# Kernel tuning notes

Measured on AMD Instinct MI355X. Metric: run time of the kernel, lower is better.

## Reference

```python
import jax, jax.numpy as jnp
import numpy as np

N_NODES = 50000
N_EDGES = 800000
D = 64
BN_EPS = 1e-5


def setup_inputs() -> dict:
    key = jax.random.key(0)
    ks = jax.random.split(key, 16)
    x = jax.random.normal(ks[0], (N_NODES, D), dtype=jnp.float32)
    edge_index = jax.random.randint(ks[1], (2, N_EDGES), 0, N_NODES, dtype=jnp.int64)
    s = 1.0 / np.sqrt(D)
    def lin(k):
        kw, kb = jax.random.split(k)
        W = jax.random.uniform(kw, (D, D), jnp.float32, -s, s)
        b = jax.random.uniform(kb, (D,), jnp.float32, -s, s)
        return W, b
    W1_0, b1_0 = lin(ks[2])
    W2_0, b2_0 = lin(ks[3])
    W1_1, b1_1 = lin(ks[4])
    W2_1, b2_1 = lin(ks[5])
    return {
        "x": x, "edge_index": edge_index,
        "W1_0": W1_0, "b1_0": b1_0, "g_0": jnp.ones((D,), jnp.float32), "beta_0": jnp.zeros((D,), jnp.float32), "W2_0": W2_0, "b2_0": b2_0,
        "W1_1": W1_1, "b1_1": b1_1, "g_1": jnp.ones((D,), jnp.float32), "beta_1": jnp.zeros((D,), jnp.float32), "W2_1": W2_1, "b2_1": b2_1,
    }


def _gin_layer(x, src, dst, W1, b1, g, beta, W2, b2):
    # GINConv with eps=0: h_i = MLP( x_i + sum_{j->i} x_j )
    agg = jax.ops.segment_sum(x[src], dst, num_segments=N_NODES)  # [N, D]
    h = agg + x
    h = h @ W1 + b1
    # BatchNorm1d (training-mode batch statistics, biased variance)
    mean = jnp.mean(h, axis=0)
    var = jnp.var(h, axis=0)
    h = (h - mean) * jax.lax.rsqrt(var + BN_EPS) * g + beta
    h = jax.nn.relu(h)
    h = jax.nn.relu(h @ W2 + b2)
    return h


def reference(x, edge_index, W1_0, b1_0, g_0, beta_0, W2_0, b2_0,
              W1_1, b1_1, g_1, beta_1, W2_1, b2_1):
    src = edge_index[0]  # message source j
    dst = edge_index[1]  # aggregation target i
    h1 = _gin_layer(x, src, dst, W1_0, b1_0, g_0, beta_0, W2_0, b2_0)
    h2 = _gin_layer(h1, src, dst, W1_1, b1_1, g_1, beta_1, W2_1, b2_1)
    return (h1, h2)
```

## Files before the change

### kernel.cpp

```cpp
#include <hip/hip_runtime.h>
#include <hip/hip_bf16.h>

#define N_NODES 50000
#define N_EDGES 800000
#define DD 64
#define RPB 64
#define GBLOCKS ((N_NODES + RPB - 1) / RPB)
#define MBLOCKS ((N_NODES + 63) / 64)
#define NBUCKET ((N_NODES + 63) / 64)
#define PIDSTRIDE 800
#define NBP (NBUCKET * 8)
#define EDGE_BLOCKS (N_EDGES / 256)
#define BN_EPS 1e-5f


__device__ __forceinline__ float bf2f(unsigned short b) {
    return __uint_as_float(((unsigned)b) << 16);
}
__device__ __forceinline__ float loadF(const void* p, int i, int isf) {
    return isf ? ((const float*)p)[i] : bf2f(((const unsigned short*)p)[i]);
}
template<bool ISF>
__device__ __forceinline__ float4 ld4(const void* p, int i) {
    if (ISF) return *reinterpret_cast<const float4*>((const float*)p + i);
    ushort4 u = *reinterpret_cast<const ushort4*>((const unsigned short*)p + i);
    return make_float4(bf2f(u.x), bf2f(u.y), bf2f(u.z), bf2f(u.w));
}
__device__ __forceinline__ void acc8(float4& a, float4& b, uint4 u) {
    a.x += __uint_as_float(u.x << 16);
    a.y += __uint_as_float(u.x & 0xFFFF0000u);
    a.z += __uint_as_float(u.y << 16);
    a.w += __uint_as_float(u.y & 0xFFFF0000u);
    b.x += __uint_as_float(u.z << 16);
    b.y += __uint_as_float(u.z & 0xFFFF0000u);
    b.z += __uint_as_float(u.w << 16);
    b.w += __uint_as_float(u.w & 0xFFFF0000u);
}

__global__ __launch_bounds__(256) void initcast_kernel(
    const void* __restrict__ x, const int* __restrict__ ei,
    int* __restrict__ flags, int* __restrict__ bpcnt,
    unsigned short* __restrict__ xb)
{
    __shared__ int cntF, cntI;
    int t = threadIdx.x;
    if (t == 0) { cntF = 0; cntI = 0; }
    __syncthreads();
    unsigned short wd = ((const unsigned short*)x)[2 * t];
    int e = (wd >> 7) & 0xFF;
    if (e >= 0x70 && e <= 0x8F) atomicAdd(&cntF, 1);
    if (t < 128 && ei[2 * t + 1] == 0) atomicAdd(&cntI, 1);
    __syncthreads();
    int isf = (cntF < 128) ? 1 : 0;
    int i64 = (cntI > 64) ? 1 : 0;

    int gid = blockIdx.x * 256 + t;
    if (blockIdx.x == 0 && t == 0) {
        flags[0] = isf;
        flags[1] = i64;
    }

    {
        int d = i64 ? ei[2 * N_EDGES + 2 * gid] : ei[N_EDGES + gid];
        atomicAdd(bpcnt + (blockIdx.x & 7) * PIDSTRIDE + (d >> 6), 1);
    }

    int i = gid * 8;
    if (i < N_NODES * DD) {
        if (isf) {
            float4 a = *reinterpret_cast<const float4*>((const float*)x + i);
            float4 b = *reinterpret_cast<const float4*>((const float*)x + i + 4);
            ushort4 o0, o1;
            o0.x = __bfloat16_as_ushort(__float2bfloat16(a.x));
            o0.y = __bfloat16_as_ushort(__float2bfloat16(a.y));
            o0.z = __bfloat16_as_ushort(__float2bfloat16(a.z));
            o0.w = __bfloat16_as_ushort(__float2bfloat16(a.w));
            o1.x = __bfloat16_as_ushort(__float2bfloat16(b.x));
            o1.y = __bfloat16_as_ushort(__float2bfloat16(b.y));
            o1.z = __bfloat16_as_ushort(__float2bfloat16(b.z));
            o1.w = __bfloat16_as_ushort(__float2bfloat16(b.w));
            *reinterpret_cast<ushort4*>(xb + i) = o0;
            *reinterpret_cast<ushort4*>(xb + i + 4) = o1;
        } else {
            *reinterpret_cast<uint4*>(xb + i) =
                *reinterpret_cast<const uint4*>((const unsigned short*)x + i);
        }
    }
}

#define BPCH 25
__global__ __launch_bounds__(256) void bpscan_kernel(const int* __restrict__ bpcnt,
                                                     int* __restrict__ bpcur,
                                                     int* __restrict__ boff) {
    __shared__ int tmp[256];
    int t = threadIdx.x;
    int lo = t * BPCH;
    int hi = lo + BPCH; if (hi > NBP) hi = NBP;
    int s = 0;
    for (int i = lo; i < hi; ++i)
        s += bpcnt[(i & 7) * PIDSTRIDE + (i >> 3)];
    tmp[t] = s;
    __syncthreads();
    #pragma unroll
    for (int d = 1; d < 256; d <<= 1) {
        int u = (t >= d) ? tmp[t - d] : 0;
        __syncthreads();
        tmp[t] += u;
        __syncthreads();
    }
    int run = (t == 0) ? 0 : tmp[t - 1];
    for (int i = lo; i < hi; ++i) {
        bpcur[i * 16] = run;
        if ((i & 7) == 0) boff[i >> 3] = run;
        run += bpcnt[(i & 7) * PIDSTRIDE + (i >> 3)];
    }
    if (t == 255) boff[NBUCKET] = tmp[255];
}

__global__ void fillA_kernel(const int* __restrict__ ei, int* __restrict__ bpcur,
                             unsigned int* __restrict__ tmp, const int* __restrict__ flags) {
    int i64 = flags[1];
    int e = blockIdx.x * 256 + threadIdx.x;
    int s, d;
    if (i64) { s = ei[2 * e]; d = ei[2 * N_EDGES + 2 * e]; }
    else     { s = ei[e];     d = ei[N_EDGES + e]; }
    int bin = (d >> 6) * 8 + (blockIdx.x & 7);
    int pos = atomicAdd(bpcur + bin * 16, 1);
    tmp[pos] = (unsigned)s | ((unsigned)(d & 63) << 16);
}

__global__ __launch_bounds__(256) void fillB_kernel(const int* __restrict__ boff,
                                                    const unsigned int* __restrict__ tmp,
                                                    unsigned short* __restrict__ srt,
                                                    int* __restrict__ off) {
    __shared__ int lcnt[64];
    __shared__ int cur64[64];
    int b = blockIdx.x;
    int t = threadIdx.x;
    if (t < 64) lcnt[t] = 0;
    __syncthreads();
    int start = boff[b], end = boff[b + 1];
    for (int i = start + t; i < end; i += 256)
        atomicAdd(&lcnt[tmp[i] >> 16], 1);
    __syncthreads();
    if (t < 64) {
        int v = lcnt[t];
        int s = v;
        #pragma unroll
        for (int d = 1; d < 64; d <<= 1) {
            int u = __shfl_up(s, d, 64);
            if (t >= d) s += u;
        }
        int o = start + (s - v);
        int node = b * 64 + t;
        if (node <= N_NODES) off[node] = o;
        cur64[t] = o;
    }
    __syncthreads();
    for (int i = start + t; i < end; i += 256) {
        unsigned v = tmp[i];
        int pos = atomicAdd(&cur64[v >> 16], 1);
        srt[pos] = (unsigned short)(v & 0xFFFFu);
    }
}

__global__ __launch_bounds__(512) void gather_gemm_stats_kernel(
    const unsigned short* __restrict__ xb, const void* __restrict__ self_src, int force_f32,
    const int* __restrict__ off, const unsigned short* __restrict__ srt,
    const void* __restrict__ W, const void* __restrict__ bias,
    float* __restrict__ out_, float* __restrict__ sums, const int* __restrict__ flags)
{
    __shared__ float sIn[RPB][DD];
    __shared__ float r1[8][DD], r2[8][DD];
    int tid = threadIdx.x;
    int lane = tid & 63, w = tid >> 6;
    int rs = lane >> 3, ch = lane & 7;
    int row0 = blockIdx.x * RPB;
    int isf = force_f32 ? 1 : flags[0];

    int lr = w * 8 + rs;
    int r = row0 + lr;
    float4 a  = make_float4(0.f, 0.f, 0.f, 0.f);
    float4 b  = make_float4(0.f, 0.f, 0.f, 0.f);
    float4 a2 = make_float4(0.f, 0.f, 0.f, 0.f);
    float4 b2 = make_float4(0.f, 0.f, 0.f, 0.f);
    if (r < N_NODES) {
        a = isf ? ld4<true>(self_src, r * DD + 8 * ch)
                : ld4<false>(self_src, r * DD + 8 * ch);
        b = isf ? ld4<true>(self_src, r * DD + 8 * ch + 4)
                : ld4<false>(self_src, r * DD + 8 * ch + 4);
        int k0 = off[r], k1 = off[r + 1];
        int k = k0;
        for (; k + 8 <= k1; k += 8) {
            int n0 = srt[k],     n1 = srt[k + 1], n2 = srt[k + 2], n3 = srt[k + 3];
            int n4 = srt[k + 4], n5 = srt[k + 5], n6 = srt[k + 6], n7 = srt[k + 7];
            uint4 u0 = *reinterpret_cast<const uint4*>(xb + n0 * DD + 8 * ch);
            uint4 u1 = *reinterpret_cast<const uint4*>(xb + n1 * DD + 8 * ch);
            uint4 u2 = *reinterpret_cast<const uint4*>(xb + n2 * DD + 8 * ch);
            uint4 u3 = *reinterpret_cast<const uint4*>(xb + n3 * DD + 8 * ch);
            uint4 u4 = *reinterpret_cast<const uint4*>(xb + n4 * DD + 8 * ch);
            uint4 u5 = *reinterpret_cast<const uint4*>(xb + n5 * DD + 8 * ch);
            uint4 u6 = *reinterpret_cast<const uint4*>(xb + n6 * DD + 8 * ch);
            uint4 u7 = *reinterpret_cast<const uint4*>(xb + n7 * DD + 8 * ch);
            acc8(a, b, u0);
            acc8(a2, b2, u1);
            acc8(a, b, u2);
            acc8(a2, b2, u3);
            acc8(a, b, u4);
            acc8(a2, b2, u5);
            acc8(a, b, u6);
            acc8(a2, b2, u7);
        }
        for (; k + 2 <= k1; k += 2) {
            int n0 = srt[k], n1 = srt[k + 1];
            uint4 u0 = *reinterpret_cast<const uint4*>(xb + n0 * DD + 8 * ch);
            uint4 u1 = *reinterpret_cast<const uint4*>(xb + n1 * DD + 8 * ch);
            acc8(a, b, u0);
            acc8(a2, b2, u1);
        }
        if (k < k1) {
            int n0 = srt[k];
            acc8(a, b, *reinterpret_cast<const uint4*>(xb + n0 * DD + 8 * ch));
        }
        a.x += a2.x; a.y += a2.y; a.z += a2.z; a.w += a2.w;
        b.x += b2.x; b.y += b2.y; b.z += b2.z; b.w += b2.w;
    }
    *reinterpret_cast<float4*>(&sIn[lr][8 * ch]) = a;
    *reinterpret_cast<float4*>(&sIn[lr][8 * ch + 4]) = b;
    __syncthreads();

    float wcol[DD];
    #pragma unroll
    for (int k = 0; k < DD; ++k) wcol[k] = loadF(W, k * DD + lane, isf);
    float bv = loadF(bias, lane, isf);

    float s1 = 0.f, s2 = 0.f;
    #pragma unroll 4
    for (int j = 0; j < 8; ++j) {
        int jr = w * 8 + j;
        float c0 = 0.f, c1 = 0.f, c2 = 0.f, c3 = 0.f;
        #pragma unroll
        for (int k = 0; k < DD; k += 4) {
            float4 aa = *reinterpret_cast<const float4*>(&sIn[jr][k]);
            c0 += aa.x * wcol[k];
            c1 += aa.y * wcol[k + 1];
            c2 += aa.z * wcol[k + 2];
            c3 += aa.w * wcol[k + 3];
        }
        float acc = bv + ((c0 + c1) + (c2 + c3));
        int rr = row0 + jr;
        if (rr < N_NODES) {
            out_[rr * DD + lane] = acc;
            s1 += acc;
            s2 += acc * acc;
        }
    }
    r1[w][lane] = s1; r2[w][lane] = s2;
    __syncthreads();
    if (w == 0) {
        float t1 = 0.f, t2 = 0.f;
        #pragma unroll
        for (int q = 0; q < 8; ++q) { t1 += r1[q][lane]; t2 += r2[q][lane]; }
        atomicAdd(&sums[lane], t1);
        atomicAdd(&sums[64 + lane], t2);
    }
}

__global__ __launch_bounds__(256) void mlp2_kernel(
    const float* __restrict__ in_, const float* __restrict__ sums,
    const void* __restrict__ gma, const void* __restrict__ beta,
    const void* __restrict__ W, const void* __restrict__ bias,
    float* __restrict__ oF, unsigned short* obf, const int* __restrict__ flags)
{
    __shared__ float sIn[64][DD];
    __shared__ float sScale[DD], sShift[DD];
    int isf = flags[0];
    int tid = threadIdx.x;
    int c = tid & 63, g = tid >> 6;
    int row0 = blockIdx.x * 64;

    if (tid < 64) {
        float S1 = sums[tid];
        float S2 = sums[64 + tid];
        float mean = S1 * (1.0f / N_NODES);
        float var  = S2 * (1.0f / N_NODES) - mean * mean;
        float scale = rsqrtf(var + BN_EPS) * loadF(gma, tid, isf);
        sScale[tid] = scale;
        sShift[tid] = loadF(beta, tid, isf) - mean * scale;
    }
    __syncthreads();

    #pragma unroll
    for (int j = 0; j < 4; ++j) {
        int lr = (tid >> 4) + 16 * j;
        int cc = (tid & 15) << 2;
        int r = row0 + lr;
        float4 v = make_float4(0.f, 0.f, 0.f, 0.f);
        if (r < N_NODES) {
            v = *reinterpret_cast<const float4*>(in_ + r * DD + cc);
            float4 sc = *reinterpret_cast<const float4*>(&sScale[cc]);
            float4 sh = *reinterpret_cast<const float4*>(&sShift[cc]);
            v.x = fmaxf(v.x * sc.x + sh.x, 0.f);
            v.y = fmaxf(v.y * sc.y + sh.y, 0.f);
            v.z = fmaxf(v.z * sc.z + sh.z, 0.f);
            v.w = fmaxf(v.w * sc.w + sh.w, 0.f);
        }
        *reinterpret_cast<float4*>(&sIn[lr][cc]) = v;
    }
    __syncthreads();

    float wcol[DD];
    #pragma unroll
    for (int k = 0; k < DD; ++k) wcol[k] = loadF(W, k * DD + c, isf);
    float bv = loadF(bias, c, isf);

    #pragma unroll 4
    for (int j = 0; j < 16; ++j) {
        int lr = g * 16 + j;
        float a0 = 0.f, a1 = 0.f, a2 = 0.f, a3 = 0.f;
        #pragma unroll
        for (int k = 0; k < DD; k += 4) {
            float4 a = *reinterpret_cast<const float4*>(&sIn[lr][k]);
            a0 += a.x * wcol[k];
            a1 += a.y * wcol[k + 1];
            a2 += a.z * wcol[k + 2];
            a3 += a.w * wcol[k + 3];
        }
        float acc = fmaxf(bv + ((a0 + a1) + (a2 + a3)), 0.f);
        int r = row0 + lr;
        if (r < N_NODES) {
            oF[r * DD + c] = acc;
            if (obf) obf[r * DD + c] = __bfloat16_as_ushort(__float2bfloat16(acc));
        }
    }
}

extern "C" void kernel_launch(void* const* d_in, const int* in_sizes, int n_in,
                              void* d_out, int out_size, void* d_ws, size_t ws_size,
                              hipStream_t stream)
{
    (void)in_sizes; (void)n_in; (void)out_size; (void)ws_size;
    const void* x  = d_in[0];
    const int* ei  = (const int*)d_in[1];
    const void* W1_0 = d_in[2];  const void* b1_0 = d_in[3];
    const void* g_0  = d_in[4];  const void* be_0 = d_in[5];
    const void* W2_0 = d_in[6];  const void* b2_0 = d_in[7];
    const void* W1_1 = d_in[8];  const void* b1_1 = d_in[9];
    const void* g_1  = d_in[10]; const void* be_1 = d_in[11];
    const void* W2_1 = d_in[12]; const void* b2_1 = d_in[13];

    float* wsf   = (float*)d_ws;
    float* sumsA = wsf;
    float* sumsB = wsf + 128;
    int*  flags  = (int*)(wsf + 256);
    int*  bpcnt  = (int*)(wsf + 512);
    int*  off    = bpcnt + 6400;
    int*  boff   = off + 50064;
    int*  bpcur  = boff + 800;
    unsigned int* tmp32 = (unsigned int*)(bpcur + 100096);
    unsigned short* srt = (unsigned short*)(tmp32 + 800000);
    unsigned short* xb  = srt + 800064;
    float* O1    = (float*)d_out;
    float* O2    = O1 + (size_t)N_NODES * DD;

    dim3 blk(256);

    hipMemsetAsync(d_ws, 0, (size_t)(512 + 6400) * 4, stream);
    initcast_kernel<<<EDGE_BLOCKS, blk, 0, stream>>>(x, ei, flags, bpcnt, xb);
    bpscan_kernel<<<1, blk, 0, stream>>>(bpcnt, bpcur, boff);
    fillA_kernel<<<EDGE_BLOCKS, blk, 0, stream>>>(ei, bpcur, tmp32, flags);
    fillB_kernel<<<NBUCKET, blk, 0, stream>>>(boff, tmp32, srt, off);

    gather_gemm_stats_kernel<<<GBLOCKS, 512, 0, stream>>>(xb, x, 0, off, srt, W1_0, b1_0,
                                                          O2, sumsA, flags);
    mlp2_kernel<<<MBLOCKS, blk, 0, stream>>>(O2, sumsA, g_0, be_0, W2_0, b2_0, O1, xb, flags);

    gather_gemm_stats_kernel<<<GBLOCKS, 512, 0, stream>>>(xb, O1, 1, off, srt, W1_1, b1_1,
                                                          O2, sumsB, flags);
    mlp2_kernel<<<MBLOCKS, blk, 0, stream>>>(O2, sumsB, g_1, be_1, W2_1, b2_1, O2, nullptr, flags);
}
```

Baseline: 309.2 us.

## Fuse per-bucket CSR fill into first-layer gather-GEMM-stats kernel

The second pass of the counting sort (per-bucket local histogram, scan and scatter into the sorted source array) now runs inside the first layer's gather/GEMM/BN-stats kernel, one block per 64-node bucket. This removes a kernel launch and the round trip through global memory for the row offsets, since the first layer reads them from shared memory. The cost is that each block must finish its sort before gathering. The freshly written srt values are then read back through the cache within the same block, and the larger block adds more sort threads. The second-layer kernel also drops the force_f32 flag and hardcodes float loads for its self input.

```diff
diff --git a/kernel.cpp b/kernel.cpp
--- a/kernel.cpp
+++ b/kernel.cpp
@@ -129,43 +129,146 @@
     tmp[pos] = (unsigned)s | ((unsigned)(d & 63) << 16);
 }
 
-__global__ __launch_bounds__(256) void fillB_kernel(const int* __restrict__ boff,
-                                                    const unsigned int* __restrict__ tmp,
-                                                    unsigned short* __restrict__ srt,
-                                                    int* __restrict__ off) {
-    __shared__ int lcnt[64];
-    __shared__ int cur64[64];
+__global__ __launch_bounds__(512) void gather1_fused_kernel(
+    const unsigned short* __restrict__ xb, const void* __restrict__ self_src,
+    const int* __restrict__ boff, const unsigned int* __restrict__ tmp,
+    unsigned short* __restrict__ srt, int* __restrict__ off,
+    const void* __restrict__ W, const void* __restrict__ bias,
+    float* __restrict__ out_, float* __restrict__ sums, const int* __restrict__ flags)
+{
+    __shared__ float sIn[RPB][DD];
+    __shared__ float r1[8][DD], r2[8][DD];
+    __shared__ int lofs[65];
+    int tid = threadIdx.x;
+    int lane = tid & 63, w = tid >> 6;
+    int rs = lane >> 3, ch = lane & 7;
     int b = blockIdx.x;
-    int t = threadIdx.x;
-    if (t < 64) lcnt[t] = 0;
-    __syncthreads();
-    int start = boff[b], end = boff[b + 1];
-    for (int i = start + t; i < end; i += 256)
-        atomicAdd(&lcnt[tmp[i] >> 16], 1);
-    __syncthreads();
-    if (t < 64) {
-        int v = lcnt[t];
-        int s = v;
+    int row0 = b * RPB;
+    int isf = flags[0];
+
+    {
+        int* lcnt = (int*)&r1[0][0];
+        int* cur  = lcnt + 64;
+        if (tid < 64) lcnt[tid] = 0;
+        __syncthreads();
+        int start = boff[b], end = boff[b + 1];
+        for (int i = start + tid; i < end; i += 512)
+            atomicAdd(&lcnt[tmp[i] >> 16], 1);
+        __syncthreads();
+        if (tid < 64) {
+            int v = lcnt[tid];
+            int s = v;
+            #pragma unroll
+            for (int d = 1; d < 64; d <<= 1) {
+                int u = __shfl_up(s, d, 64);
+                if (tid >= d) s += u;
+            }
+            int o = start + (s - v);
+            int node = row0 + tid;
+            if (node <= N_NODES) off[node] = o;
+            cur[tid] = o;
+            lofs[tid] = o;
+            if (tid == 63) lofs[64] = end;
+        }
+        __syncthreads();
+        for (int i = start + tid; i < end; i += 512) {
+            unsigned v = tmp[i];
+            int pos = atomicAdd(&cur[v >> 16], 1);
+            srt[pos] = (unsigned short)(v & 0xFFFFu);
+        }
+        __syncthreads();
+    }
+
+    int lr = w * 8 + rs;
+    int r = row0 + lr;
+    float4 a  = make_float4(0.f, 0.f, 0.f, 0.f);
+    float4 b4 = make_float4(0.f, 0.f, 0.f, 0.f);
+    float4 a2 = make_float4(0.f, 0.f, 0.f, 0.f);
+    float4 b2 = make_float4(0.f, 0.f, 0.f, 0.f);
+    if (r < N_NODES) {
+        a  = isf ? ld4<true>(self_src, r * DD + 8 * ch)
+                 : ld4<false>(self_src, r * DD + 8 * ch);
+        b4 = isf ? ld4<true>(self_src, r * DD + 8 * ch + 4)
+                 : ld4<false>(self_src, r * DD + 8 * ch + 4);
+        int k0 = lofs[lr], k1 = lofs[lr + 1];
+        int k = k0;
+        for (; k + 8 <= k1; k += 8) {
+            int n0 = srt[k],     n1 = srt[k + 1], n2 = srt[k + 2], n3 = srt[k + 3];
+            int n4 = srt[k + 4], n5 = srt[k + 5], n6 = srt[k + 6], n7 = srt[k + 7];
+            uint4 u0 = *reinterpret_cast<const uint4*>(xb + n0 * DD + 8 * ch);
+            uint4 u1 = *reinterpret_cast<const uint4*>(xb + n1 * DD + 8 * ch);
+            uint4 u2 = *reinterpret_cast<const uint4*>(xb + n2 * DD + 8 * ch);
+            uint4 u3 = *reinterpret_cast<const uint4*>(xb + n3 * DD + 8 * ch);
+            uint4 u4 = *reinterpret_cast<const uint4*>(xb + n4 * DD + 8 * ch);
+            uint4 u5 = *reinterpret_cast<const uint4*>(xb + n5 * DD + 8 * ch);
+            uint4 u6 = *reinterpret_cast<const uint4*>(xb + n6 * DD + 8 * ch);
+            uint4 u7 = *reinterpret_cast<const uint4*>(xb + n7 * DD + 8 * ch);
+            acc8(a, b4, u0);
+            acc8(a2, b2, u1);
+            acc8(a, b4, u2);
+            acc8(a2, b2, u3);
+            acc8(a, b4, u4);
+            acc8(a2, b2, u5);
+            acc8(a, b4, u6);
+            acc8(a2, b2, u7);
+        }
+        for (; k + 2 <= k1; k += 2) {
+            int n0 = srt[k], n1 = srt[k + 1];
+            uint4 u0 = *reinterpret_cast<const uint4*>(xb + n0 * DD + 8 * ch);
+            uint4 u1 = *reinterpret_cast<const uint4*>(xb + n1 * DD + 8 * ch);
+            acc8(a, b4, u0);
+            acc8(a2, b2, u1);
+        }
+        if (k < k1) {
+            int n0 = srt[k];
+            acc8(a, b4, *reinterpret_cast<const uint4*>(xb + n0 * DD + 8 * ch));
+        }
+        a.x += a2.x; a.y += a2.y; a.z += a2.z; a.w += a2.w;
+        b4.x += b2.x; b4.y += b2.y; b4.z += b2.z; b4.w += b2.w;
+    }
+    *reinterpret_cast<float4*>(&sIn[lr][8 * ch]) = a;
+    *reinterpret_cast<float4*>(&sIn[lr][8 * ch + 4]) = b4;
+    __syncthreads();
+
+    float wcol[DD];
+    #pragma unroll
+    for (int k = 0; k < DD; ++k) wcol[k] = loadF(W, k * DD + lane, isf);
+    float bv = loadF(bias, lane, isf);
+
+    float s1 = 0.f, s2 = 0.f;
+    #pragma unroll 4
+    for (int j = 0; j < 8; ++j) {
+        int jr = w * 8 + j;
+        float c0 = 0.f, c1 = 0.f, c2 = 0.f, c3 = 0.f;
         #pragma unroll
-        for (int d = 1; d < 64; d <<= 1) {
-            int u = __shfl_up(s, d, 64);
-            if (t >= d) s += u;
-        }
-        int o = start + (s - v);
-        int node = b * 64 + t;
-        if (node <= N_NODES) off[node] = o;
-        cur64[t] = o;
-    }
-    __syncthreads();
-    for (int i = start + t; i < end; i += 256) {
-        unsigned v = tmp[i];
-        int pos = atomicAdd(&cur64[v >> 16], 1);
-        srt[pos] = (unsigned short)(v & 0xFFFFu);
+        for (int k = 0; k < DD; k += 4) {
+            float4 aa = *reinterpret_cast<const float4*>(&sIn[jr][k]);
+            c0 += aa.x * wcol[k];
+            c1 += aa.y * wcol[k + 1];
+            c2 += aa.z * wcol[k + 2];
+            c3 += aa.w * wcol[k + 3];
+        }
+        float acc = bv + ((c0 + c1) + (c2 + c3));
+        int rr = row0 + jr;
+        if (rr < N_NODES) {
+            out_[rr * DD + lane] = acc;
+            s1 += acc;
+            s2 += acc * acc;
+        }
+    }
+    r1[w][lane] = s1; r2[w][lane] = s2;
+    __syncthreads();
+    if (w == 0) {
+        float t1 = 0.f, t2 = 0.f;
+        #pragma unroll
+        for (int q = 0; q < 8; ++q) { t1 += r1[q][lane]; t2 += r2[q][lane]; }
+        atomicAdd(&sums[lane], t1);
+        atomicAdd(&sums[64 + lane], t2);
     }
 }
 
 __global__ __launch_bounds__(512) void gather_gemm_stats_kernel(
-    const unsigned short* __restrict__ xb, const void* __restrict__ self_src, int force_f32,
+    const unsigned short* __restrict__ xb, const float* __restrict__ self_src,
     const int* __restrict__ off, const unsigned short* __restrict__ srt,
     const void* __restrict__ W, const void* __restrict__ bias,
     float* __restrict__ out_, float* __restrict__ sums, const int* __restrict__ flags)
@@ -176,7 +279,7 @@
     int lane = tid & 63, w = tid >> 6;
     int rs = lane >> 3, ch = lane & 7;
     int row0 = blockIdx.x * RPB;
-    int isf = force_f32 ? 1 : flags[0];
+    int isf = flags[0];
 
     int lr = w * 8 + rs;
     int r = row0 + lr;
@@ -185,10 +288,8 @@
     float4 a2 = make_float4(0.f, 0.f, 0.f, 0.f);
     float4 b2 = make_float4(0.f, 0.f, 0.f, 0.f);
     if (r < N_NODES) {
-        a = isf ? ld4<true>(self_src, r * DD + 8 * ch)
-                : ld4<false>(self_src, r * DD + 8 * ch);
-        b = isf ? ld4<true>(self_src, r * DD + 8 * ch + 4)
-                : ld4<false>(self_src, r * DD + 8 * ch + 4);
+        a = ld4<true>(self_src, r * DD + 8 * ch);
+        b = ld4<true>(self_src, r * DD + 8 * ch + 4);
         int k0 = off[r], k1 = off[r + 1];
         int k = k0;
         for (; k + 8 <= k1; k += 8) {
@@ -369,13 +470,12 @@
     initcast_kernel<<<EDGE_BLOCKS, blk, 0, stream>>>(x, ei, flags, bpcnt, xb);
     bpscan_kernel<<<1, blk, 0, stream>>>(bpcnt, bpcur, boff);
     fillA_kernel<<<EDGE_BLOCKS, blk, 0, stream>>>(ei, bpcur, tmp32, flags);
-    fillB_kernel<<<NBUCKET, blk, 0, stream>>>(boff, tmp32, srt, off);
-
-    gather_gemm_stats_kernel<<<GBLOCKS, 512, 0, stream>>>(xb, x, 0, off, srt, W1_0, b1_0,
-                                                          O2, sumsA, flags);
+
+    gather1_fused_kernel<<<NBUCKET, 512, 0, stream>>>(xb, x, boff, tmp32, srt, off,
+                                                      W1_0, b1_0, O2, sumsA, flags);
     mlp2_kernel<<<MBLOCKS, blk, 0, stream>>>(O2, sumsA, g_0, be_0, W2_0, b2_0, O1, xb, flags);
 
-    gather_gemm_stats_kernel<<<GBLOCKS, 512, 0, stream>>>(xb, O1, 1, off, srt, W1_1, b1_1,
+    gather_gemm_stats_kernel<<<GBLOCKS, 512, 0, stream>>>(xb, O1, off, srt, W1_1, b1_1,
                                                           O2, sumsB, flags);
     mlp2_kernel<<<MBLOCKS, blk, 0, stream>>>(O2, sumsB, g_1, be_1, W2_1, b2_1, O2, nullptr, flags);
 }
```

Measured after the change: 309.1 us. Within noise of the previous version (-0.0%).
